# Optimization experiments

Hardware: AMD Instinct MI355X
Metric: run time of the kernel (lower is better)

Reference implementation:

```python
import jax, jax.numpy as jnp
import numpy as np

V, D, HID, HEADS = 50000, 128, 128, 4
N, E, G = 100000, 1600000, 256
CH = HID // HEADS  # per-head channels for layer 1


def setup_inputs() -> dict:
    key = jax.random.key(0)
    ks = jax.random.split(key, 16)
    g = lambda i, shape, scale=0.05: jax.random.normal(ks[i], shape, jnp.float32) * scale
    return {
        "x_lex": jax.random.randint(ks[0], (N,), 0, V),
        "edge_index": jax.random.randint(ks[1], (2, E), 0, N),
        "batch": jnp.sort(jax.random.randint(ks[2], (N,), 0, G)),
        "emb": g(3, (V, D)),
        "W1": g(4, (D, HID)), "a1_src": g(5, (HEADS, CH)), "a1_dst": g(6, (HEADS, CH)), "b1": jnp.zeros((HID,), jnp.float32),
        "W2": g(7, (HID, HID)), "a2_src": g(8, (1, HID)), "a2_dst": g(9, (1, HID)), "b2": jnp.zeros((HID,), jnp.float32),
        "Wc1": g(10, (HID, HID // 2)), "bc1": jnp.zeros((HID // 2,), jnp.float32),
        "Wc2": g(11, (HID // 2, 1)), "bc2": jnp.zeros((1,), jnp.float32),
    }


def gat_layer(x, src, dst, W, a_src, a_dst, b, heads, ch):
    """PyG-style GATConv (v1), concat=True, negative_slope=0.2."""
    n = x.shape[0]
    h = (x @ W).reshape(n, heads, ch)                 # [N,H,C]
    al_s = (h * a_src).sum(-1)                        # [N,H]
    al_d = (h * a_dst).sum(-1)                        # [N,H]
    e = jax.nn.leaky_relu(al_s[src] + al_d[dst], 0.2) # [Etot,H]
    # segment softmax over incoming edges per destination node
    m = jax.ops.segment_max(e, dst, num_segments=n)
    ex = jnp.exp(e - m[dst])
    s = jax.ops.segment_sum(ex, dst, num_segments=n)
    alpha = ex / s[dst]
    out = jax.ops.segment_sum(alpha[:, :, None] * h[src], dst, num_segments=n)  # [N,H,C]
    return out.reshape(n, heads * ch) + b


def reference(x_lex, edge_index, batch, emb, W1, a1_src, a1_dst, b1, W2, a2_src, a2_dst, b2, Wc1, bc1, Wc2, bc2):
    n = x_lex.shape[0]
    loops = jnp.arange(n)  # GATConv adds self-loops by default
    src = jnp.concatenate([edge_index[0], loops])
    dst = jnp.concatenate([edge_index[1], loops])
    x = emb[x_lex]                                               # [N,D]
    h = jax.nn.elu(gat_layer(x, src, dst, W1, a1_src, a1_dst, b1, HEADS, CH))
    h = jax.nn.elu(gat_layer(h, src, dst, W2, a2_src, a2_dst, b2, 1, HID))
    sums = jax.ops.segment_sum(h, batch, num_segments=G)
    cnt = jax.ops.segment_sum(jnp.ones((n,), h.dtype), batch, num_segments=G)
    h_pool = sums / jnp.maximum(cnt, 1.0)[:, None]               # global mean pool [G,HID]
    logits = jax.nn.relu(h_pool @ Wc1 + bc1) @ Wc2 + bc2         # [G,1]
    return (logits, h_pool)
```

## Files before the change

kernel.cpp:

```cpp
#include <hip/hip_runtime.h>
#include <hip/hip_bf16.h>
#include <math.h>

#define P_CHUNK 8192
#define NBKT 1024
#define CAP  4096

typedef float f4 __attribute__((ext_vector_type(4)));

__device__ __forceinline__ float lrelu(float x){ return x < 0.f ? 0.2f*x : x; }
__device__ __forceinline__ float elu_(float x){ return x > 0.f ? x : expm1f(x); }

__global__ __launch_bounds__(256) void p3scatter(const int* __restrict__ ei, int E, int Etot,
                                                 int* __restrict__ bcur, int* __restrict__ tmp){
  __shared__ int lh[NBKT];
  __shared__ int lbase[NBKT];
  int tid = threadIdx.x;
  for (int t = tid; t < NBKT; t += 256) lh[t] = 0;
  __syncthreads();
  int base = blockIdx.x * P_CHUNK;
  for (int j = 0; j < P_CHUNK; j += 256){
    int i = base + j + tid;
    if (i < Etot){
      int dst = (i < E) ? ei[E + i] : (i - E);
      atomicAdd(&lh[dst >> 7], 1);
    }
  }
  __syncthreads();
  for (int t = tid; t < NBKT; t += 256){
    int v = lh[t];
    lbase[t] = v ? atomicAdd(&bcur[t], v) : 0;
  }
  __syncthreads();
  for (int t = tid; t < NBKT; t += 256) lh[t] = 0;
  __syncthreads();
  for (int j = 0; j < P_CHUNK; j += 256){
    int i = base + j + tid;
    if (i < Etot){
      int s, d;
      if (i < E){ s = ei[i]; d = ei[E + i]; } else { s = i - E; d = i - E; }
      int b = d >> 7;
      int r = atomicAdd(&lh[b], 1);
      tmp[b*CAP + lbase[b] + r] = s | ((d & 127) << 17);
    }
  }
}

__global__ __launch_bounds__(256) void p2scan(const int* __restrict__ bcur,
                                              int* __restrict__ bbase,
                                              int Etot, int* __restrict__ off, int N){
  __shared__ int wsum[4];
  __shared__ int runsh;
  int tid = threadIdx.x, lane = tid & 63, w = tid >> 6;
  if (tid == 0) runsh = 0;
  __syncthreads();
  for (int c = 0; c < NBKT; c += 256){
    int v = bcur[c + tid];
    int x = v;
    #pragma unroll
    for (int d = 1; d < 64; d <<= 1){ int y = __shfl_up(x, d); if (lane >= d) x += y; }
    if (lane == 63) wsum[w] = x;
    __syncthreads();
    int wpre = 0;
    for (int i = 0; i < w; i++) wpre += wsum[i];
    int run = runsh;
    bbase[c + tid] = run + wpre + x - v;
    __syncthreads();
    if (tid == 0) runsh = run + wsum[0] + wsum[1] + wsum[2] + wsum[3];
    __syncthreads();
  }
  if (tid == 0) off[N] = Etot;
}

__global__ __launch_bounds__(256) void p4local(const int* __restrict__ tmp,
                                               const int* __restrict__ bbase,
                                               const int* __restrict__ bcnt,
                                               int* __restrict__ off, int* __restrict__ srcs, int N){
  __shared__ int cnt[128];
  __shared__ int offL[128];
  int b = blockIdx.x, tid = threadIdx.x;
  int e0 = bbase[b];
  int ne = bcnt[b];
  const int* slab = tmp + (size_t)b*CAP;
  if (tid < 128) cnt[tid] = 0;
  __syncthreads();
  for (int j = tid; j < ne; j += 256)
    atomicAdd(&cnt[(slab[j] >> 17) & 127], 1);
  __syncthreads();
  if (tid < 64){
    int v0 = cnt[2*tid], v1 = cnt[2*tid + 1];
    int p = v0 + v1;
    int x = p;
    #pragma unroll
    for (int d = 1; d < 64; d <<= 1){ int y = __shfl_up(x, d); if (tid >= d) x += y; }
    int excl = x - p;
    offL[2*tid]     = excl;
    offL[2*tid + 1] = excl + v0;
  }
  __syncthreads();
  if (tid < 128){
    int gd = b*128 + tid;
    if (gd < N) off[gd] = e0 + offL[tid];
    cnt[tid] = 0;
  }
  __syncthreads();
  for (int j = tid; j < ne; j += 256){
    int e = slab[j];
    int d = (e >> 17) & 127;
    int r = atomicAdd(&cnt[d], 1);
    srcs[e0 + offL[d] + r] = e & 0x1FFFF;
  }
}

template<int H, bool GATHER>
__global__ __launch_bounds__(256) void gemm_al(
    const float* __restrict__ X, const int* __restrict__ idx,
    const float* __restrict__ W, const float* __restrict__ asrc,
    const float* __restrict__ adst, float* __restrict__ Hout,
    float* __restrict__ als, float* __restrict__ ald, int n)
{
  __shared__ float xs[128][68];
  __shared__ float wch[32][128];
  int tid = threadIdx.x;
  int tr = tid >> 5, tc = tid & 31;
  int r8 = tr*8, c4 = tc*4;
  int row0 = blockIdx.x * 64;

  #pragma unroll
  for (int j=0;j<8;j++){
    int e = tid + j*256;
    int r = e >> 5, cq = e & 31;
    int gr = row0 + r;
    float4 v = make_float4(0.f,0.f,0.f,0.f);
    if (gr < n){
      int srow = GATHER ? idx[gr] : gr;
      v = *reinterpret_cast<const float4*>(&X[(size_t)srow*128 + cq*4]);
    }
    xs[cq*4+0][r] = v.x;
    xs[cq*4+1][r] = v.y;
    xs[cq*4+2][r] = v.z;
    xs[cq*4+3][r] = v.w;
  }

  float acc[8][4];
  #pragma unroll
  for (int r=0;r<8;r++)
    #pragma unroll
    for (int i=0;i<4;i++) acc[r][i] = 0.f;

  for (int kc=0;kc<4;kc++){
    __syncthreads();
    #pragma unroll
    for (int j=0;j<4;j++){
      int e = tid + j*256;
      int r = e>>5, cq = e&31;
      *reinterpret_cast<float4*>(&wch[r][cq*4]) =
        *reinterpret_cast<const float4*>(&W[(size_t)(kc*32+r)*128 + cq*4]);
    }
    __syncthreads();
    #pragma unroll
    for (int kk=0;kk<32;kk++){
      int k = kc*32+kk;
      const float4 x0 = *reinterpret_cast<const float4*>(&xs[k][r8]);
      const float4 x1 = *reinterpret_cast<const float4*>(&xs[k][r8+4]);
      const float4 wv = *reinterpret_cast<const float4*>(&wch[kk][c4]);
      acc[0][0]=fmaf(x0.x,wv.x,acc[0][0]); acc[0][1]=fmaf(x0.x,wv.y,acc[0][1]);
      acc[0][2]=fmaf(x0.x,wv.z,acc[0][2]); acc[0][3]=fmaf(x0.x,wv.w,acc[0][3]);
      acc[1][0]=fmaf(x0.y,wv.x,acc[1][0]); acc[1][1]=fmaf(x0.y,wv.y,acc[1][1]);
      acc[1][2]=fmaf(x0.y,wv.z,acc[1][2]); acc[1][3]=fmaf(x0.y,wv.w,acc[1][3]);
      acc[2][0]=fmaf(x0.z,wv.x,acc[2][0]); acc[2][1]=fmaf(x0.z,wv.y,acc[2][1]);
      acc[2][2]=fmaf(x0.z,wv.z,acc[2][2]); acc[2][3]=fmaf(x0.z,wv.w,acc[2][3]);
      acc[3][0]=fmaf(x0.w,wv.x,acc[3][0]); acc[3][1]=fmaf(x0.w,wv.y,acc[3][1]);
      acc[3][2]=fmaf(x0.w,wv.z,acc[3][2]); acc[3][3]=fmaf(x0.w,wv.w,acc[3][3]);
      acc[4][0]=fmaf(x1.x,wv.x,acc[4][0]); acc[4][1]=fmaf(x1.x,wv.y,acc[4][1]);
      acc[4][2]=fmaf(x1.x,wv.z,acc[4][2]); acc[4][3]=fmaf(x1.x,wv.w,acc[4][3]);
      acc[5][0]=fmaf(x1.y,wv.x,acc[5][0]); acc[5][1]=fmaf(x1.y,wv.y,acc[5][1]);
      acc[5][2]=fmaf(x1.y,wv.z,acc[5][2]); acc[5][3]=fmaf(x1.y,wv.w,acc[5][3]);
      acc[6][0]=fmaf(x1.z,wv.x,acc[6][0]); acc[6][1]=fmaf(x1.z,wv.y,acc[6][1]);
      acc[6][2]=fmaf(x1.z,wv.z,acc[6][2]); acc[6][3]=fmaf(x1.z,wv.w,acc[6][3]);
      acc[7][0]=fmaf(x1.w,wv.x,acc[7][0]); acc[7][1]=fmaf(x1.w,wv.y,acc[7][1]);
      acc[7][2]=fmaf(x1.w,wv.z,acc[7][2]); acc[7][3]=fmaf(x1.w,wv.w,acc[7][3]);
    }
  }

  const float4 asv = *reinterpret_cast<const float4*>(&asrc[c4]);
  const float4 adv = *reinterpret_cast<const float4*>(&adst[c4]);
  const int GT = 32 / H;
  int hh = tc / GT;

  #pragma unroll
  for (int r=0;r<8;r++){
    int gr = row0 + r8 + r;
    if (gr < n){
      *reinterpret_cast<float4*>(&Hout[(size_t)gr*128 + c4]) =
        make_float4(acc[r][0], acc[r][1], acc[r][2], acc[r][3]);
    }
    float ps = acc[r][0]*asv.x + acc[r][1]*asv.y + acc[r][2]*asv.z + acc[r][3]*asv.w;
    float pd = acc[r][0]*adv.x + acc[r][1]*adv.y + acc[r][2]*adv.z + acc[r][3]*adv.w;
    #pragma unroll
    for (int m=1;m<GT;m<<=1){ ps += __shfl_xor(ps,m); pd += __shfl_xor(pd,m); }
    if ((tc & (GT-1)) == 0 && gr < n){
      als[(size_t)gr*H + hh] = ps;
      ald[(size_t)gr*H + hh] = pd;
    }
  }
}

template<int H>
__global__ __launch_bounds__(256) void aggr(
    const float* __restrict__ h, const float* __restrict__ als,
    const float* __restrict__ ald, const int* __restrict__ srcs,
    const int* __restrict__ off, const float* __restrict__ bias,
    float* __restrict__ out, int n)
{
  __shared__ float s_p[4][64*H];
  __shared__ int   s_s[4][64];
  int tid = threadIdx.x;
  int wid = tid >> 6, lane = tid & 63;
  int d = blockIdx.x*4 + wid;
  if (d >= n) return;
  int half = lane >> 5, ch = lane & 31;
  int c4 = ch*4;
  const int hh = (H==1) ? 0 : (ch >> 3);

  int s0 = off[d], s1 = off[d+1];

  float adv[H];
  #pragma unroll
  for (int q=0;q<H;q++) adv[q] = ald[(size_t)d*H + q];

  float m[H], ssum[H];
  #pragma unroll
  for (int q=0;q<H;q++){ m[q] = -INFINITY; ssum[q] = 0.f; }
  float a0=0.f, a1=0.f, a2=0.f, a3=0.f;

  for (int base = s0; base < s1; base += 64){
    int cl = s1 - base; if (cl > 64) cl = 64;

    int sv = 0;
    float e[H];
    if (lane < cl){
      sv = srcs[base + lane];
      #pragma unroll
      for (int q=0;q<H;q++) e[q] = lrelu(als[(size_t)sv*H + q] + adv[q]);
    } else {
      #pragma unroll
      for (int q=0;q<H;q++) e[q] = -INFINITY;
    }

    float cm[H];
    #pragma unroll
    for (int q=0;q<H;q++) cm[q] = e[q];
    #pragma unroll
    for (int sh=1; sh<64; sh<<=1){
      #pragma unroll
      for (int q=0;q<H;q++) cm[q] = fmaxf(cm[q], __shfl_xor(cm[q], sh));
    }

    float p[H], sc[H];
    #pragma unroll
    for (int q=0;q<H;q++){
      float nm = fmaxf(m[q], cm[q]);
      sc[q] = __expf(m[q] - nm);
      ssum[q] *= sc[q];
      m[q] = nm;
      p[q] = __expf(e[q] - nm);
    }
    float schh = sc[0];
    #pragma unroll
    for (int q=1;q<H;q++) schh = (hh==q) ? sc[q] : schh;
    a0 *= schh; a1 *= schh; a2 *= schh; a3 *= schh;

    float cs[H];
    #pragma unroll
    for (int q=0;q<H;q++) cs[q] = p[q];
    #pragma unroll
    for (int sh=1; sh<64; sh<<=1){
      #pragma unroll
      for (int q=0;q<H;q++) cs[q] += __shfl_xor(cs[q], sh);
    }
    #pragma unroll
    for (int q=0;q<H;q++) ssum[q] += cs[q];

    #pragma unroll
    for (int q=0;q<H;q++) s_p[wid][lane*H + q] = p[q];
    s_s[wid][lane] = sv;

    for (int j = half; j < cl; j += 2){
      int s = s_s[wid][j];
      float w = s_p[wid][j*H + hh];
      const float4 hv = *reinterpret_cast<const float4*>(&h[(size_t)s*128 + c4]);
      a0 = fmaf(w, hv.x, a0);
      a1 = fmaf(w, hv.y, a1);
      a2 = fmaf(w, hv.z, a2);
      a3 = fmaf(w, hv.w, a3);
    }
  }

  a0 += __shfl_xor(a0, 32);
  a1 += __shfl_xor(a1, 32);
  a2 += __shfl_xor(a2, 32);
  a3 += __shfl_xor(a3, 32);

  float den = ssum[0];
  #pragma unroll
  for (int q=1;q<H;q++) den = (hh==q) ? ssum[q] : den;
  float inv = 1.f / den;

  if (half == 0){
    const float4 bv = *reinterpret_cast<const float4*>(&bias[c4]);
    float4 o;
    o.x = elu_(a0*inv + bv.x);
    o.y = elu_(a1*inv + bv.y);
    o.z = elu_(a2*inv + bv.z);
    o.w = elu_(a3*inv + bv.w);
    *reinterpret_cast<float4*>(&out[(size_t)d*128 + c4]) = o;
  }
}

__global__ __launch_bounds__(256) void kpool(const float* __restrict__ act,
    const int* __restrict__ batch, int n, float* __restrict__ pool)
{
  __shared__ int sb[2];
  __shared__ float part[128];
  int g = blockIdx.x, tid = threadIdx.x;
  if (tid == 0){
    int lo=0, hi=n;
    while (lo<hi){ int mid=(lo+hi)>>1; if (batch[mid] < g) lo=mid+1; else hi=mid; }
    sb[0]=lo;
    int lo2=lo, hi2=n;
    while (lo2<hi2){ int mid=(lo2+hi2)>>1; if (batch[mid] < g+1) lo2=mid+1; else hi2=mid; }
    sb[1]=lo2;
  }
  __syncthreads();
  int lo=sb[0], hi=sb[1];
  int c = tid & 127, half = tid >> 7;
  float acc = 0.f;
  for (int i=lo+half; i<hi; i+=2) acc += act[(size_t)i*128 + c];
  if (half == 0) part[c] = acc;
  __syncthreads();
  if (half == 1) part[c] += acc;
  __syncthreads();
  if (half == 0){
    float cnt = (float)(hi-lo);
    pool[(size_t)g*128 + c] = part[c] / fmaxf(cnt, 1.f);
  }
}

__global__ __launch_bounds__(64) void kclassify(const float* __restrict__ pool,
    const float* __restrict__ Wc1, const float* __restrict__ bc1,
    const float* __restrict__ Wc2, const float* __restrict__ bc2,
    float* __restrict__ logits)
{
  int g = blockIdx.x, j = threadIdx.x;
  const float* hp = pool + (size_t)g*128;
  float t = bc1[j];
  #pragma unroll 8
  for (int c=0;c<128;c++) t = fmaf(hp[c], Wc1[c*64+j], t);
  t = fmaxf(t, 0.f) * Wc2[j];
  for (int m=1;m<64;m<<=1) t += __shfl_xor(t, m);
  if (j==0) logits[g] = t + bc2[0];
}

extern "C" void kernel_launch(void* const* d_in, const int* in_sizes, int n_in,
                              void* d_out, int out_size, void* d_ws, size_t ws_size,
                              hipStream_t stream)
{
  const int*   x_lex = (const int*)d_in[0];
  const int*   ei    = (const int*)d_in[1];
  const int*   batch = (const int*)d_in[2];
  const float* emb   = (const float*)d_in[3];
  const float* W1    = (const float*)d_in[4];
  const float* a1s   = (const float*)d_in[5];
  const float* a1d   = (const float*)d_in[6];
  const float* b1    = (const float*)d_in[7];
  const float* W2    = (const float*)d_in[8];
  const float* a2s   = (const float*)d_in[9];
  const float* a2d   = (const float*)d_in[10];
  const float* b2    = (const float*)d_in[11];
  const float* Wc1   = (const float*)d_in[12];
  const float* bc1   = (const float*)d_in[13];
  const float* Wc2   = (const float*)d_in[14];
  const float* bc2   = (const float*)d_in[15];

  int N = in_sizes[0];
  int E = in_sizes[1] / 2;
  int Etot = E + N;
  const int G = 256;

  char* p = (char*)d_ws;
  float* hbuf   = (float*)p;          p += (size_t)N*128*4;
  float* act    = (float*)p;          p += (size_t)N*128*4;
  float* als    = (float*)p;          p += (size_t)N*4*4;
  float* ald    = (float*)p;          p += (size_t)N*4*4;
  int*   off    = (int*)p;            p += (size_t)(N+1)*4;
  int*   srcs   = (int*)p;            p += (size_t)Etot*4;
  int*   bbase  = (int*)p;            p += (NBKT+1)*4;
  int*   bcur   = (int*)p;
  int*   tmp    = (int*)hbuf;

  hipMemsetAsync(bcur, 0, NBKT*4, stream);
  int nblk = (Etot + P_CHUNK - 1) / P_CHUNK;
  int nb   = (N + 127) / 128;
  p3scatter<<<nblk,256,0,stream>>>(ei, E, Etot, bcur, tmp);
  p2scan   <<<1,   256,0,stream>>>(bcur, bbase, Etot, off, N);
  p4local  <<<nb,  256,0,stream>>>(tmp, bbase, bcur, off, srcs, N);

  int gb = (N + 63)/64;
  gemm_al<4,true ><<<gb,256,0,stream>>>(emb, x_lex, W1, a1s, a1d, hbuf, als, ald, N);
  aggr<4><<<(N+3)/4,256,0,stream>>>(hbuf, als, ald, srcs, off, b1, act, N);

  gemm_al<1,false><<<gb,256,0,stream>>>(act, nullptr, W2, a2s, a2d, hbuf, als, ald, N);
  aggr<1><<<(N+3)/4,256,0,stream>>>(hbuf, als, ald, srcs, off, b2, act, N);

  float* out = (float*)d_out;
  kpool<<<G,256,0,stream>>>(act, batch, N, out + G);
  kclassify<<<G,64,0,stream>>>(out + G, Wc1, bc1, Wc2, bc2, out);
}
```

Baseline: 516.6 us.

## Restructure GEMM to row-major LDS with direct W loads; 4-way edge split in aggregation

The GEMM kernel now stores X tiles row-major in shared memory and reads W directly from global memory (served from cache) instead of staging W chunks through shared memory. This removes the transposed scatter stores and the per-chunk barriers. The aggregation kernel now has each lane handle 8 channels with 4 edge groups per wave instead of 2, so more neighbor rows are in flight at once, at the cost of extra shuffle reductions. Risks are more global/L2 traffic for W, LDS bank conflicts on the row-major reads, and higher register use.

```diff
diff --git a/kernel.cpp b/kernel.cpp
--- a/kernel.cpp
+++ b/kernel.cpp
@@ -119,8 +119,7 @@
     const float* __restrict__ adst, float* __restrict__ Hout,
     float* __restrict__ als, float* __restrict__ ald, int n)
 {
-  __shared__ float xs[128][68];
-  __shared__ float wch[32][128];
+  __shared__ float xs[64][132];
   int tid = threadIdx.x;
   int tr = tid >> 5, tc = tid & 31;
   int r8 = tr*8, c4 = tc*4;
@@ -131,16 +130,14 @@
     int e = tid + j*256;
     int r = e >> 5, cq = e & 31;
     int gr = row0 + r;
-    float4 v = make_float4(0.f,0.f,0.f,0.f);
+    f4 v = (f4)(0.f);
     if (gr < n){
       int srow = GATHER ? idx[gr] : gr;
-      v = *reinterpret_cast<const float4*>(&X[(size_t)srow*128 + cq*4]);
-    }
-    xs[cq*4+0][r] = v.x;
-    xs[cq*4+1][r] = v.y;
-    xs[cq*4+2][r] = v.z;
-    xs[cq*4+3][r] = v.w;
-  }
+      v = *reinterpret_cast<const f4*>(&X[(size_t)srow*128 + cq*4]);
+    }
+    *reinterpret_cast<f4*>(&xs[r][cq*4]) = v;
+  }
+  __syncthreads();
 
   float acc[8][4];
   #pragma unroll
@@ -148,43 +145,25 @@
     #pragma unroll
     for (int i=0;i<4;i++) acc[r][i] = 0.f;
 
-  for (int kc=0;kc<4;kc++){
-    __syncthreads();
-    #pragma unroll
-    for (int j=0;j<4;j++){
-      int e = tid + j*256;
-      int r = e>>5, cq = e&31;
-      *reinterpret_cast<float4*>(&wch[r][cq*4]) =
-        *reinterpret_cast<const float4*>(&W[(size_t)(kc*32+r)*128 + cq*4]);
-    }
-    __syncthreads();
-    #pragma unroll
-    for (int kk=0;kk<32;kk++){
-      int k = kc*32+kk;
-      const float4 x0 = *reinterpret_cast<const float4*>(&xs[k][r8]);
-      const float4 x1 = *reinterpret_cast<const float4*>(&xs[k][r8+4]);
-      const float4 wv = *reinterpret_cast<const float4*>(&wch[kk][c4]);
-      acc[0][0]=fmaf(x0.x,wv.x,acc[0][0]); acc[0][1]=fmaf(x0.x,wv.y,acc[0][1]);
-      acc[0][2]=fmaf(x0.x,wv.z,acc[0][2]); acc[0][3]=fmaf(x0.x,wv.w,acc[0][3]);
-      acc[1][0]=fmaf(x0.y,wv.x,acc[1][0]); acc[1][1]=fmaf(x0.y,wv.y,acc[1][1]);
-      acc[1][2]=fmaf(x0.y,wv.z,acc[1][2]); acc[1][3]=fmaf(x0.y,wv.w,acc[1][3]);
-      acc[2][0]=fmaf(x0.z,wv.x,acc[2][0]); acc[2][1]=fmaf(x0.z,wv.y,acc[2][1]);
-      acc[2][2]=fmaf(x0.z,wv.z,acc[2][2]); acc[2][3]=fmaf(x0.z,wv.w,acc[2][3]);
-      acc[3][0]=fmaf(x0.w,wv.x,acc[3][0]); acc[3][1]=fmaf(x0.w,wv.y,acc[3][1]);
-      acc[3][2]=fmaf(x0.w,wv.z,acc[3][2]); acc[3][3]=fmaf(x0.w,wv.w,acc[3][3]);
-      acc[4][0]=fmaf(x1.x,wv.x,acc[4][0]); acc[4][1]=fmaf(x1.x,wv.y,acc[4][1]);
-      acc[4][2]=fmaf(x1.x,wv.z,acc[4][2]); acc[4][3]=fmaf(x1.x,wv.w,acc[4][3]);
-      acc[5][0]=fmaf(x1.y,wv.x,acc[5][0]); acc[5][1]=fmaf(x1.y,wv.y,acc[5][1]);
-      acc[5][2]=fmaf(x1.y,wv.z,acc[5][2]); acc[5][3]=fmaf(x1.y,wv.w,acc[5][3]);
-      acc[6][0]=fmaf(x1.z,wv.x,acc[6][0]); acc[6][1]=fmaf(x1.z,wv.y,acc[6][1]);
-      acc[6][2]=fmaf(x1.z,wv.z,acc[6][2]); acc[6][3]=fmaf(x1.z,wv.w,acc[6][3]);
-      acc[7][0]=fmaf(x1.w,wv.x,acc[7][0]); acc[7][1]=fmaf(x1.w,wv.y,acc[7][1]);
-      acc[7][2]=fmaf(x1.w,wv.z,acc[7][2]); acc[7][3]=fmaf(x1.w,wv.w,acc[7][3]);
-    }
-  }
-
-  const float4 asv = *reinterpret_cast<const float4*>(&asrc[c4]);
-  const float4 adv = *reinterpret_cast<const float4*>(&adst[c4]);
+  #pragma unroll 4
+  for (int kq=0;kq<32;kq++){
+    int k0 = kq*4;
+    f4 xv[8], wv[4];
+    #pragma unroll
+    for (int i=0;i<8;i++) xv[i] = *reinterpret_cast<const f4*>(&xs[r8+i][k0]);
+    #pragma unroll
+    for (int kk=0;kk<4;kk++) wv[kk] = *reinterpret_cast<const f4*>(&W[(size_t)(k0+kk)*128 + c4]);
+    #pragma unroll
+    for (int kk=0;kk<4;kk++)
+      #pragma unroll
+      for (int i=0;i<8;i++)
+        #pragma unroll
+        for (int j=0;j<4;j++)
+          acc[i][j] = fmaf(xv[i][kk], wv[kk][j], acc[i][j]);
+  }
+
+  const f4 asv = *reinterpret_cast<const f4*>(&asrc[c4]);
+  const f4 adv = *reinterpret_cast<const f4*>(&adst[c4]);
   const int GT = 32 / H;
   int hh = tc / GT;
 
@@ -192,11 +171,11 @@
   for (int r=0;r<8;r++){
     int gr = row0 + r8 + r;
     if (gr < n){
-      *reinterpret_cast<float4*>(&Hout[(size_t)gr*128 + c4]) =
-        make_float4(acc[r][0], acc[r][1], acc[r][2], acc[r][3]);
-    }
-    float ps = acc[r][0]*asv.x + acc[r][1]*asv.y + acc[r][2]*asv.z + acc[r][3]*asv.w;
-    float pd = acc[r][0]*adv.x + acc[r][1]*adv.y + acc[r][2]*adv.z + acc[r][3]*adv.w;
+      f4 o = { acc[r][0], acc[r][1], acc[r][2], acc[r][3] };
+      *reinterpret_cast<f4*>(&Hout[(size_t)gr*128 + c4]) = o;
+    }
+    float ps = acc[r][0]*asv[0] + acc[r][1]*asv[1] + acc[r][2]*asv[2] + acc[r][3]*asv[3];
+    float pd = acc[r][0]*adv[0] + acc[r][1]*adv[1] + acc[r][2]*adv[2] + acc[r][3]*adv[3];
     #pragma unroll
     for (int m=1;m<GT;m<<=1){ ps += __shfl_xor(ps,m); pd += __shfl_xor(pd,m); }
     if ((tc & (GT-1)) == 0 && gr < n){
@@ -219,20 +198,22 @@
   int wid = tid >> 6, lane = tid & 63;
   int d = blockIdx.x*4 + wid;
   if (d >= n) return;
-  int half = lane >> 5, ch = lane & 31;
-  int c4 = ch*4;
-  const int hh = (H==1) ? 0 : (ch >> 3);
+  int q = lane >> 4, ch16 = lane & 15;
+  int c8 = ch16 * 8;
+  const int hh = (H==1) ? 0 : (ch16 >> 2);
 
   int s0 = off[d], s1 = off[d+1];
 
   float adv[H];
   #pragma unroll
-  for (int q=0;q<H;q++) adv[q] = ald[(size_t)d*H + q];
+  for (int qq=0;qq<H;qq++) adv[qq] = ald[(size_t)d*H + qq];
 
   float m[H], ssum[H];
   #pragma unroll
-  for (int q=0;q<H;q++){ m[q] = -INFINITY; ssum[q] = 0.f; }
-  float a0=0.f, a1=0.f, a2=0.f, a3=0.f;
+  for (int qq=0;qq<H;qq++){ m[qq] = -INFINITY; ssum[qq] = 0.f; }
+  float a[8];
+  #pragma unroll
+  for (int i=0;i<8;i++) a[i] = 0.f;
 
   for (int base = s0; base < s1; base += 64){
     int cl = s1 - base; if (cl > 64) cl = 64;
@@ -242,79 +223,92 @@
     if (lane < cl){
       sv = srcs[base + lane];
       #pragma unroll
-      for (int q=0;q<H;q++) e[q] = lrelu(als[(size_t)sv*H + q] + adv[q]);
+      for (int qq=0;qq<H;qq++) e[qq] = lrelu(als[(size_t)sv*H + qq] + adv[qq]);
     } else {
       #pragma unroll
-      for (int q=0;q<H;q++) e[q] = -INFINITY;
+      for (int qq=0;qq<H;qq++) e[qq] = -INFINITY;
     }
 
     float cm[H];
     #pragma unroll
-    for (int q=0;q<H;q++) cm[q] = e[q];
+    for (int qq=0;qq<H;qq++) cm[qq] = e[qq];
     #pragma unroll
     for (int sh=1; sh<64; sh<<=1){
       #pragma unroll
-      for (int q=0;q<H;q++) cm[q] = fmaxf(cm[q], __shfl_xor(cm[q], sh));
+      for (int qq=0;qq<H;qq++) cm[qq] = fmaxf(cm[qq], __shfl_xor(cm[qq], sh));
     }
 
     float p[H], sc[H];
     #pragma unroll
-    for (int q=0;q<H;q++){
-      float nm = fmaxf(m[q], cm[q]);
-      sc[q] = __expf(m[q] - nm);
-      ssum[q] *= sc[q];
-      m[q] = nm;
-      p[q] = __expf(e[q] - nm);
+    for (int qq=0;qq<H;qq++){
+      float nm = fmaxf(m[qq], cm[qq]);
+      sc[qq] = __expf(m[qq] - nm);
+      ssum[qq] *= sc[qq];
+      m[qq] = nm;
+      p[qq] = __expf(e[qq] - nm);
     }
     float schh = sc[0];
     #pragma unroll
-    for (int q=1;q<H;q++) schh = (hh==q) ? sc[q] : schh;
-    a0 *= schh; a1 *= schh; a2 *= schh; a3 *= schh;
+    for (int qq=1;qq<H;qq++) schh = (hh==qq) ? sc[qq] : schh;
+    #pragma unroll
+    for (int i=0;i<8;i++) a[i] *= schh;
 
     float cs[H];
     #pragma unroll
-    for (int q=0;q<H;q++) cs[q] = p[q];
+    for (int qq=0;qq<H;qq++) cs[qq] = p[qq];
     #pragma unroll
     for (int sh=1; sh<64; sh<<=1){
       #pragma unroll
-      for (int q=0;q<H;q++) cs[q] += __shfl_xor(cs[q], sh);
-    }
-    #pragma unroll
-    for (int q=0;q<H;q++) ssum[q] += cs[q];
-
-    #pragma unroll
-    for (int q=0;q<H;q++) s_p[wid][lane*H + q] = p[q];
+      for (int qq=0;qq<H;qq++) cs[qq] += __shfl_xor(cs[qq], sh);
+    }
+    #pragma unroll
+    for (int qq=0;qq<H;qq++) ssum[qq] += cs[qq];
+
+    #pragma unroll
+    for (int qq=0;qq<H;qq++) s_p[wid][lane*H + qq] = p[qq];
     s_s[wid][lane] = sv;
 
-    for (int j = half; j < cl; j += 2){
+    for (int j = q; j < cl; j += 4){
       int s = s_s[wid][j];
       float w = s_p[wid][j*H + hh];
-      const float4 hv = *reinterpret_cast<const float4*>(&h[(size_t)s*128 + c4]);
-      a0 = fmaf(w, hv.x, a0);
-      a1 = fmaf(w, hv.y, a1);
-      a2 = fmaf(w, hv.z, a2);
-      a3 = fmaf(w, hv.w, a3);
-    }
-  }
-
-  a0 += __shfl_xor(a0, 32);
-  a1 += __shfl_xor(a1, 32);
-  a2 += __shfl_xor(a2, 32);
-  a3 += __shfl_xor(a3, 32);
+      const f4 hv0 = *reinterpret_cast<const f4*>(&h[(size_t)s*128 + c8]);
+      const f4 hv1 = *reinterpret_cast<const f4*>(&h[(size_t)s*128 + c8 + 4]);
+      a[0] = fmaf(w, hv0[0], a[0]);
+      a[1] = fmaf(w, hv0[1], a[1]);
+      a[2] = fmaf(w, hv0[2], a[2]);
+      a[3] = fmaf(w, hv0[3], a[3]);
+      a[4] = fmaf(w, hv1[0], a[4]);
+      a[5] = fmaf(w, hv1[1], a[5]);
+      a[6] = fmaf(w, hv1[2], a[6]);
+      a[7] = fmaf(w, hv1[3], a[7]);
+    }
+  }
+
+  #pragma unroll
+  for (int i=0;i<8;i++){
+    a[i] += __shfl_xor(a[i], 16);
+    a[i] += __shfl_xor(a[i], 32);
+  }
 
   float den = ssum[0];
   #pragma unroll
-  for (int q=1;q<H;q++) den = (hh==q) ? ssum[q] : den;
+  for (int qq=1;qq<H;qq++) den = (hh==qq) ? ssum[qq] : den;
   float inv = 1.f / den;
 
-  if (half == 0){
-    const float4 bv = *reinterpret_cast<const float4*>(&bias[c4]);
-    float4 o;
-    o.x = elu_(a0*inv + bv.x);
-    o.y = elu_(a1*inv + bv.y);
-    o.z = elu_(a2*inv + bv.z);
-    o.w = elu_(a3*inv + bv.w);
-    *reinterpret_cast<float4*>(&out[(size_t)d*128 + c4]) = o;
+  if (q == 0){
+    const f4 bv0 = *reinterpret_cast<const f4*>(&bias[c8]);
+    const f4 bv1 = *reinterpret_cast<const f4*>(&bias[c8 + 4]);
+    f4 o0, o1;
+    o0[0] = elu_(a[0]*inv + bv0[0]);
+    o0[1] = elu_(a[1]*inv + bv0[1]);
+    o0[2] = elu_(a[2]*inv + bv0[2]);
+    o0[3] = elu_(a[3]*inv + bv0[3]);
+    o1[0] = elu_(a[4]*inv + bv1[0]);
+    o1[1] = elu_(a[5]*inv + bv1[1]);
+    o1[2] = elu_(a[6]*inv + bv1[2]);
+    o1[3] = elu_(a[7]*inv + bv1[3]);
+    *reinterpret_cast<f4*>(&out[(size_t)d*128 + c8])     = o0;
+    *reinterpret_cast<f4*>(&out[(size_t)d*128 + c8 + 4]) = o1;
   }
 }
 
```

Result: no change. 511.7 us (-1.0%).

## Store GEMM input tile row-major with rotated swizzle, read W directly from global

Applied to the files above, without the earlier changes.

The GEMM+attention-logit kernel now stores the 64x128 input tile row-major in shared memory with a rotating column swizzle, instead of a transposed layout built from scalar stores. The four shared-memory staging passes for W, and their barriers, are removed. Each thread now reads W rows directly from global memory (cache-resident) as float4 loads and does an outer product over 4 k-values per step. This cuts LDS store traffic and synchronisation. The cost is more global or L1 loads of W per thread and more LDS reads per FMA for the x operand.

```diff
diff --git a/kernel.cpp b/kernel.cpp
--- a/kernel.cpp
+++ b/kernel.cpp
@@ -119,8 +119,7 @@
     const float* __restrict__ adst, float* __restrict__ Hout,
     float* __restrict__ als, float* __restrict__ ald, int n)
 {
-  __shared__ float xs[128][68];
-  __shared__ float wch[32][128];
+  __shared__ float xs[64][128];
   int tid = threadIdx.x;
   int tr = tid >> 5, tc = tid & 31;
   int r8 = tr*8, c4 = tc*4;
@@ -131,16 +130,14 @@
     int e = tid + j*256;
     int r = e >> 5, cq = e & 31;
     int gr = row0 + r;
-    float4 v = make_float4(0.f,0.f,0.f,0.f);
+    f4 v = (f4)(0.f);
     if (gr < n){
       int srow = GATHER ? idx[gr] : gr;
-      v = *reinterpret_cast<const float4*>(&X[(size_t)srow*128 + cq*4]);
-    }
-    xs[cq*4+0][r] = v.x;
-    xs[cq*4+1][r] = v.y;
-    xs[cq*4+2][r] = v.z;
-    xs[cq*4+3][r] = v.w;
-  }
+      v = *reinterpret_cast<const f4*>(&X[(size_t)srow*128 + cq*4]);
+    }
+    *reinterpret_cast<f4*>(&xs[r][(cq*4 + 4*r) & 127]) = v;
+  }
+  __syncthreads();
 
   float acc[8][4];
   #pragma unroll
@@ -148,43 +145,28 @@
     #pragma unroll
     for (int i=0;i<4;i++) acc[r][i] = 0.f;
 
-  for (int kc=0;kc<4;kc++){
-    __syncthreads();
-    #pragma unroll
-    for (int j=0;j<4;j++){
-      int e = tid + j*256;
-      int r = e>>5, cq = e&31;
-      *reinterpret_cast<float4*>(&wch[r][cq*4]) =
-        *reinterpret_cast<const float4*>(&W[(size_t)(kc*32+r)*128 + cq*4]);
-    }
-    __syncthreads();
-    #pragma unroll
-    for (int kk=0;kk<32;kk++){
-      int k = kc*32+kk;
-      const float4 x0 = *reinterpret_cast<const float4*>(&xs[k][r8]);
-      const float4 x1 = *reinterpret_cast<const float4*>(&xs[k][r8+4]);
-      const float4 wv = *reinterpret_cast<const float4*>(&wch[kk][c4]);
-      acc[0][0]=fmaf(x0.x,wv.x,acc[0][0]); acc[0][1]=fmaf(x0.x,wv.y,acc[0][1]);
-      acc[0][2]=fmaf(x0.x,wv.z,acc[0][2]); acc[0][3]=fmaf(x0.x,wv.w,acc[0][3]);
-      acc[1][0]=fmaf(x0.y,wv.x,acc[1][0]); acc[1][1]=fmaf(x0.y,wv.y,acc[1][1]);
-      acc[1][2]=fmaf(x0.y,wv.z,acc[1][2]); acc[1][3]=fmaf(x0.y,wv.w,acc[1][3]);
-      acc[2][0]=fmaf(x0.z,wv.x,acc[2][0]); acc[2][1]=fmaf(x0.z,wv.y,acc[2][1]);
-      acc[2][2]=fmaf(x0.z,wv.z,acc[2][2]); acc[2][3]=fmaf(x0.z,wv.w,acc[2][3]);
-      acc[3][0]=fmaf(x0.w,wv.x,acc[3][0]); acc[3][1]=fmaf(x0.w,wv.y,acc[3][1]);
-      acc[3][2]=fmaf(x0.w,wv.z,acc[3][2]); acc[3][3]=fmaf(x0.w,wv.w,acc[3][3]);
-      acc[4][0]=fmaf(x1.x,wv.x,acc[4][0]); acc[4][1]=fmaf(x1.x,wv.y,acc[4][1]);
-      acc[4][2]=fmaf(x1.x,wv.z,acc[4][2]); acc[4][3]=fmaf(x1.x,wv.w,acc[4][3]);
-      acc[5][0]=fmaf(x1.y,wv.x,acc[5][0]); acc[5][1]=fmaf(x1.y,wv.y,acc[5][1]);
-      acc[5][2]=fmaf(x1.y,wv.z,acc[5][2]); acc[5][3]=fmaf(x1.y,wv.w,acc[5][3]);
-      acc[6][0]=fmaf(x1.z,wv.x,acc[6][0]); acc[6][1]=fmaf(x1.z,wv.y,acc[6][1]);
-      acc[6][2]=fmaf(x1.z,wv.z,acc[6][2]); acc[6][3]=fmaf(x1.z,wv.w,acc[6][3]);
-      acc[7][0]=fmaf(x1.w,wv.x,acc[7][0]); acc[7][1]=fmaf(x1.w,wv.y,acc[7][1]);
-      acc[7][2]=fmaf(x1.w,wv.z,acc[7][2]); acc[7][3]=fmaf(x1.w,wv.w,acc[7][3]);
-    }
-  }
-
-  const float4 asv = *reinterpret_cast<const float4*>(&asrc[c4]);
-  const float4 adv = *reinterpret_cast<const float4*>(&adst[c4]);
+  #pragma unroll 4
+  for (int kq=0;kq<32;kq++){
+    int k0 = kq*4;
+    f4 xv[8], wv[4];
+    #pragma unroll
+    for (int i=0;i<8;i++){
+      int rr = r8 + i;
+      xv[i] = *reinterpret_cast<const f4*>(&xs[rr][(k0 + 4*rr) & 127]);
+    }
+    #pragma unroll
+    for (int kk=0;kk<4;kk++) wv[kk] = *reinterpret_cast<const f4*>(&W[(size_t)(k0+kk)*128 + c4]);
+    #pragma unroll
+    for (int kk=0;kk<4;kk++)
+      #pragma unroll
+      for (int i=0;i<8;i++)
+        #pragma unroll
+        for (int j=0;j<4;j++)
+          acc[i][j] = fmaf(xv[i][kk], wv[kk][j], acc[i][j]);
+  }
+
+  const f4 asv = *reinterpret_cast<const f4*>(&asrc[c4]);
+  const f4 adv = *reinterpret_cast<const f4*>(&adst[c4]);
   const int GT = 32 / H;
   int hh = tc / GT;
 
@@ -192,11 +174,11 @@
   for (int r=0;r<8;r++){
     int gr = row0 + r8 + r;
     if (gr < n){
-      *reinterpret_cast<float4*>(&Hout[(size_t)gr*128 + c4]) =
-        make_float4(acc[r][0], acc[r][1], acc[r][2], acc[r][3]);
-    }
-    float ps = acc[r][0]*asv.x + acc[r][1]*asv.y + acc[r][2]*asv.z + acc[r][3]*asv.w;
-    float pd = acc[r][0]*adv.x + acc[r][1]*adv.y + acc[r][2]*adv.z + acc[r][3]*adv.w;
+      f4 o = { acc[r][0], acc[r][1], acc[r][2], acc[r][3] };
+      *reinterpret_cast<f4*>(&Hout[(size_t)gr*128 + c4]) = o;
+    }
+    float ps = acc[r][0]*asv[0] + acc[r][1]*asv[1] + acc[r][2]*asv[2] + acc[r][3]*asv[3];
+    float pd = acc[r][0]*adv[0] + acc[r][1]*adv[1] + acc[r][2]*adv[2] + acc[r][3]*adv[3];
     #pragma unroll
     for (int m=1;m<GT;m<<=1){ ps += __shfl_xor(ps,m); pd += __shfl_xor(pd,m); }
     if ((tc & (GT-1)) == 0 && gr < n){
```

After: 522.7 us. Within noise of the previous version (+1.2%).
